# Optimization experiments

Measured on AMD Instinct MI355X. Metric: run time of the kernel, lower is better.

Reference implementation:

```python
import jax, jax.numpy as jnp
import numpy as np

B, T, D, H = 4, 2048, 1024, 8
HD = D // H
RES_SCALE = 1.0 / np.sqrt(2.0 * 2)  # layer_idx = 2


def rmsnorm(x, w, eps=1e-6):
    return w * (x * jax.lax.rsqrt(jnp.mean(x * x, axis=-1, keepdims=True) + eps))


def l2norm(x, eps=1e-6):
    return x * jax.lax.rsqrt(jnp.sum(x * x, axis=-1, keepdims=True) + eps)


def setup_inputs() -> dict:
    key = jax.random.key(0)
    ks = jax.random.split(key, 16)
    s = 0.02
    return {
        'x': jax.random.normal(ks[0], (B, T, D), dtype=jnp.float32),
        'ln1_w': jnp.ones((D,), jnp.float32),
        'qw': jax.random.normal(ks[1], (D, D), jnp.float32) * s,
        'kw': jax.random.normal(ks[2], (D, D), jnp.float32) * s,
        'vw': jax.random.normal(ks[3], (D, D), jnp.float32) * s,
        'bw': jax.random.normal(ks[4], (D, H), jnp.float32) * s,
        'aw': jax.random.normal(ks[5], (D, H), jnp.float32) * s,
        'A_log': jnp.log(jax.random.uniform(ks[6], (H,), jnp.float32, 1.0, 16.0)),
        'dt_bias': jnp.zeros((H,), jnp.float32),
        'gw': jax.random.normal(ks[7], (D, D), jnp.float32) * s,
        'onorm_w': jnp.ones((HD,), jnp.float32),
        'ow': jax.random.normal(ks[8], (D, D), jnp.float32) * s,
        'ln2_w': jnp.ones((D,), jnp.float32),
        'fcw': jax.random.normal(ks[9], (D, 4 * D), jnp.float32) * s,
        'pw': jax.random.normal(ks[10], (4 * D, D), jnp.float32) * s,
    }


def reference(x, ln1_w, qw, kw, vw, bw, aw, A_log, dt_bias, gw, onorm_w, ow, ln2_w, fcw, pw):
    b, t, d = x.shape
    h = rmsnorm(x, ln1_w)
    # projections: SiLU + L2-norm on q/k, SiLU on v (gated delta rule)
    q = l2norm(jax.nn.silu(h @ qw).reshape(b, t, H, HD))
    k = l2norm(jax.nn.silu(h @ kw).reshape(b, t, H, HD))
    v = jax.nn.silu(h @ vw).reshape(b, t, H, HD)
    beta = jax.nn.sigmoid(h @ bw)                                   # [b,t,H]
    g = -jnp.exp(A_log) * jax.nn.softplus(h @ aw + dt_bias)         # [b,t,H] (<=0)

    # time-major for scan
    qs, ks_, vs = (a.transpose(1, 0, 2, 3) for a in (q, k, v))
    bs, gs = beta.transpose(1, 0, 2), g.transpose(1, 0, 2)

    def step(S, inp):
        q_t, k_t, v_t, b_t, g_t = inp
        Sg = jnp.exp(g_t)[..., None, None] * S                      # decay  [b,H,dk,dv]
        kS = jnp.einsum('bhk,bhkv->bhv', k_t, Sg)                   # k^T S
        S = Sg + jnp.einsum('bhk,bhv->bhkv', b_t[..., None] * k_t, v_t - kS)
        o_t = jnp.einsum('bhk,bhkv->bhv', q_t, S)
        return S, o_t

    S0 = jnp.zeros((b, H, HD, HD), x.dtype)
    S_f, os = jax.lax.scan(step, S0, (qs, ks_, vs, bs, gs))
    o = os.transpose(1, 0, 2, 3)                                    # [b,t,H,HD]

    # use_gate: per-head RMSNorm then SiLU output gate
    gate = jax.nn.silu((h @ gw).reshape(b, t, H, HD))
    o = rmsnorm(o, onorm_w) * gate
    o = o.reshape(b, t, d) @ ow

    x1 = x + o * RES_SCALE
    h2 = rmsnorm(x1, ln2_w)
    y = x1 + (jax.nn.silu(h2 @ fcw) @ pw) * RES_SCALE
    return y, S_f
```

## Files before the change

### kernel.cpp

```cpp
#include <hip/hip_runtime.h>
#include <math.h>


#define B_ 4
#define T_ 2048
#define D_ 1024
#define H_ 8
#define HD_ 128
#define RES_SCALE 0.5f

typedef __bf16 bf16x8 __attribute__((ext_vector_type(8)));
typedef float f32x4 __attribute__((ext_vector_type(4)));

__device__ __forceinline__ float bf2f(unsigned short u) {
    union { unsigned int i; float f; } w; w.i = ((unsigned int)u) << 16; return w.f;
}
__device__ __forceinline__ unsigned short f2bf(float f) {
    unsigned int x = __float_as_uint(f);
    x += 0x7fffu + ((x >> 16) & 1u);
    return (unsigned short)(x >> 16);
}
__device__ __forceinline__ float sigm(float x) { return 1.f / (1.f + __expf(-x)); }

__global__ __launch_bounds__(256) void cvt_kernel(const float* __restrict__ src,
                                                  unsigned short* __restrict__ dst, int n4) {
    int i = blockIdx.x * 256 + threadIdx.x;
    if (i < n4) {
        float4 v = ((const float4*)src)[i];
        ushort4 o;
        o.x = f2bf(v.x); o.y = f2bf(v.y); o.z = f2bf(v.z); o.w = f2bf(v.w);
        ((ushort4*)dst)[i] = o;
    }
}

__global__ __launch_bounds__(256) void cvt2_kernel(const float* __restrict__ src,
                                                   unsigned short* __restrict__ hi,
                                                   unsigned short* __restrict__ lo, int n4) {
    int i = blockIdx.x * 256 + threadIdx.x;
    if (i < n4) {
        float4 v = ((const float4*)src)[i];
        ushort4 h, l;
        h.x = f2bf(v.x); l.x = f2bf(v.x - bf2f(h.x));
        h.y = f2bf(v.y); l.y = f2bf(v.y - bf2f(h.y));
        h.z = f2bf(v.z); l.z = f2bf(v.z - bf2f(h.z));
        h.w = f2bf(v.w); l.w = f2bf(v.w - bf2f(h.w));
        ((ushort4*)hi)[i] = h;
        ((ushort4*)lo)[i] = l;
    }
}

__global__ __launch_bounds__(256) void rmsnorm_kernel(const float* __restrict__ x,
                                                      const float* __restrict__ w,
                                                      unsigned short* __restrict__ outh,
                                                      unsigned short* __restrict__ outl) {
    int row = blockIdx.x;
    int tid = threadIdx.x;
    float4 v = ((const float4*)(x + (size_t)row * D_))[tid];
    float ss = v.x * v.x + v.y * v.y + v.z * v.z + v.w * v.w;
    #pragma unroll
    for (int m = 1; m < 64; m <<= 1) ss += __shfl_xor(ss, m);
    __shared__ float red[4];
    if ((tid & 63) == 0) red[tid >> 6] = ss;
    __syncthreads();
    float tot = red[0] + red[1] + red[2] + red[3];
    float sc = rsqrtf(tot * (1.f / D_) + 1e-6f);
    float4 wv = ((const float4*)w)[tid];
    float h0 = v.x * sc * wv.x, h1 = v.y * sc * wv.y;
    float h2 = v.z * sc * wv.z, h3 = v.w * sc * wv.w;
    ushort4 oh;
    oh.x = f2bf(h0); oh.y = f2bf(h1); oh.z = f2bf(h2); oh.w = f2bf(h3);
    ((ushort4*)(outh + (size_t)row * D_))[tid] = oh;
    if (outl) {
        ushort4 ol;
        ol.x = f2bf(h0 - bf2f(oh.x));
        ol.y = f2bf(h1 - bf2f(oh.y));
        ol.z = f2bf(h2 - bf2f(oh.z));
        ol.w = f2bf(h3 - bf2f(oh.w));
        ((ushort4*)(outl + (size_t)row * D_))[tid] = ol;
    }
}

#define LDT 40
__global__ __launch_bounds__(256) void gemm_kernel(const unsigned short* __restrict__ A,
                                                   const unsigned short* __restrict__ Bm,
                                                   unsigned short* __restrict__ Obf,
                                                   float* __restrict__ Of,
                                                   const float* __restrict__ aux,
                                                   int N, int K, int epi) {
    __shared__ unsigned short As[128 * LDT];
    __shared__ unsigned short Bs[128 * LDT];
    int tid = threadIdx.x;
    int lane = tid & 63, wave = tid >> 6;
    int wm = (wave >> 1) * 64, wn = (wave & 1) * 64;
    int l15 = lane & 15, kg = lane >> 4;
    size_t gm = blockIdx.x, gn = blockIdx.y;

    int arow0 = tid >> 2, aseg = (tid & 3) * 8;
    int brow0 = tid >> 4, bc8 = (tid & 15) * 8;

    f32x4 acc[4][4] = {};

    for (int kt = 0; kt < K; kt += 32) {
        uint4 a0 = *(const uint4*)(A + (size_t)(gm * 128 + arow0) * K + kt + aseg);
        uint4 a1 = *(const uint4*)(A + (size_t)(gm * 128 + arow0 + 64) * K + kt + aseg);
        uint4 b0 = *(const uint4*)(Bm + (size_t)(kt + brow0) * N + gn * 128 + bc8);
        uint4 b1 = *(const uint4*)(Bm + (size_t)(kt + brow0 + 16) * N + gn * 128 + bc8);
        __syncthreads();
        *(uint4*)&As[arow0 * LDT + aseg] = a0;
        *(uint4*)&As[(arow0 + 64) * LDT + aseg] = a1;
        {
            unsigned int uu[4] = {b0.x, b0.y, b0.z, b0.w};
            #pragma unroll
            for (int p = 0; p < 4; p++) {
                Bs[(bc8 + 2 * p) * LDT + brow0] = (unsigned short)(uu[p] & 0xffffu);
                Bs[(bc8 + 2 * p + 1) * LDT + brow0] = (unsigned short)(uu[p] >> 16);
            }
            unsigned int vv[4] = {b1.x, b1.y, b1.z, b1.w};
            #pragma unroll
            for (int p = 0; p < 4; p++) {
                Bs[(bc8 + 2 * p) * LDT + brow0 + 16] = (unsigned short)(vv[p] & 0xffffu);
                Bs[(bc8 + 2 * p + 1) * LDT + brow0 + 16] = (unsigned short)(vv[p] >> 16);
            }
        }
        __syncthreads();
        bf16x8 af[4], bfr[4];
        #pragma unroll
        for (int m = 0; m < 4; m++)
            af[m] = *(const bf16x8*)&As[(wm + m * 16 + l15) * LDT + kg * 8];
        #pragma unroll
        for (int n = 0; n < 4; n++)
            bfr[n] = *(const bf16x8*)&Bs[(wn + n * 16 + l15) * LDT + kg * 8];
        #pragma unroll
        for (int m = 0; m < 4; m++)
            #pragma unroll
            for (int n = 0; n < 4; n++)
                acc[m][n] = __builtin_amdgcn_mfma_f32_16x16x32_bf16(af[m], bfr[n], acc[m][n], 0, 0, 0);
    }

    #pragma unroll
    for (int m = 0; m < 4; m++) {
        #pragma unroll
        for (int n = 0; n < 4; n++) {
            #pragma unroll
            for (int j = 0; j < 4; j++) {
                size_t row = gm * 128 + wm + m * 16 + kg * 4 + j;
                size_t col = gn * 128 + wn + n * 16 + l15;
                size_t idx = row * N + col;
                float v = acc[m][n][j];
                if (epi == 0) {
                    Obf[idx] = f2bf(v * sigm(v));
                } else {
                    Of[idx] = aux[idx] + v * RES_SCALE;
                }
            }
        }
    }
}

__global__ __launch_bounds__(256) void gemm32_kernel(const unsigned short* __restrict__ Ah,
                                                     const unsigned short* __restrict__ Al,
                                                     const unsigned short* __restrict__ Bh,
                                                     const unsigned short* __restrict__ Bl,
                                                     float* __restrict__ Of,
                                                     int N, int K) {
    __shared__ unsigned short Ash[128 * LDT];
    __shared__ unsigned short Asl[128 * LDT];
    __shared__ unsigned short Bsh[128 * LDT];
    __shared__ unsigned short Bsl[128 * LDT];
    int tid = threadIdx.x;
    int lane = tid & 63, wave = tid >> 6;
    int wm = (wave >> 1) * 64, wn = (wave & 1) * 64;
    int l15 = lane & 15, kg = lane >> 4;
    size_t gm = blockIdx.x, gn = blockIdx.y;

    int arow0 = tid >> 2, aseg = (tid & 3) * 8;
    int brow0 = tid >> 4, bc8 = (tid & 15) * 8;

    f32x4 acc[4][4] = {};

    for (int kt = 0; kt < K; kt += 32) {
        size_t aoff0 = (size_t)(gm * 128 + arow0) * K + kt + aseg;
        size_t aoff1 = (size_t)(gm * 128 + arow0 + 64) * K + kt + aseg;
        size_t boff0 = (size_t)(kt + brow0) * N + gn * 128 + bc8;
        size_t boff1 = (size_t)(kt + brow0 + 16) * N + gn * 128 + bc8;
        uint4 a0h = *(const uint4*)(Ah + aoff0);
        uint4 a1h = *(const uint4*)(Ah + aoff1);
        uint4 a0l = *(const uint4*)(Al + aoff0);
        uint4 a1l = *(const uint4*)(Al + aoff1);
        uint4 b0h = *(const uint4*)(Bh + boff0);
        uint4 b1h = *(const uint4*)(Bh + boff1);
        uint4 b0l = *(const uint4*)(Bl + boff0);
        uint4 b1l = *(const uint4*)(Bl + boff1);
        __syncthreads();
        *(uint4*)&Ash[arow0 * LDT + aseg] = a0h;
        *(uint4*)&Ash[(arow0 + 64) * LDT + aseg] = a1h;
        *(uint4*)&Asl[arow0 * LDT + aseg] = a0l;
        *(uint4*)&Asl[(arow0 + 64) * LDT + aseg] = a1l;
        {
            unsigned int uu[4];
            uu[0] = b0h.x; uu[1] = b0h.y; uu[2] = b0h.z; uu[3] = b0h.w;
            #pragma unroll
            for (int p = 0; p < 4; p++) {
                Bsh[(bc8 + 2 * p) * LDT + brow0] = (unsigned short)(uu[p] & 0xffffu);
                Bsh[(bc8 + 2 * p + 1) * LDT + brow0] = (unsigned short)(uu[p] >> 16);
            }
            uu[0] = b1h.x; uu[1] = b1h.y; uu[2] = b1h.z; uu[3] = b1h.w;
            #pragma unroll
            for (int p = 0; p < 4; p++) {
                Bsh[(bc8 + 2 * p) * LDT + brow0 + 16] = (unsigned short)(uu[p] & 0xffffu);
                Bsh[(bc8 + 2 * p + 1) * LDT + brow0 + 16] = (unsigned short)(uu[p] >> 16);
            }
            uu[0] = b0l.x; uu[1] = b0l.y; uu[2] = b0l.z; uu[3] = b0l.w;
            #pragma unroll
            for (int p = 0; p < 4; p++) {
                Bsl[(bc8 + 2 * p) * LDT + brow0] = (unsigned short)(uu[p] & 0xffffu);
                Bsl[(bc8 + 2 * p + 1) * LDT + brow0] = (unsigned short)(uu[p] >> 16);
            }
            uu[0] = b1l.x; uu[1] = b1l.y; uu[2] = b1l.z; uu[3] = b1l.w;
            #pragma unroll
            for (int p = 0; p < 4; p++) {
                Bsl[(bc8 + 2 * p) * LDT + brow0 + 16] = (unsigned short)(uu[p] & 0xffffu);
                Bsl[(bc8 + 2 * p + 1) * LDT + brow0 + 16] = (unsigned short)(uu[p] >> 16);
            }
        }
        __syncthreads();
        bf16x8 afh[4], afl[4], bfh[4], bfl[4];
        #pragma unroll
        for (int m = 0; m < 4; m++) {
            afh[m] = *(const bf16x8*)&Ash[(wm + m * 16 + l15) * LDT + kg * 8];
            afl[m] = *(const bf16x8*)&Asl[(wm + m * 16 + l15) * LDT + kg * 8];
        }
        #pragma unroll
        for (int n = 0; n < 4; n++) {
            bfh[n] = *(const bf16x8*)&Bsh[(wn + n * 16 + l15) * LDT + kg * 8];
            bfl[n] = *(const bf16x8*)&Bsl[(wn + n * 16 + l15) * LDT + kg * 8];
        }
        #pragma unroll
        for (int m = 0; m < 4; m++) {
            #pragma unroll
            for (int n = 0; n < 4; n++) {
                acc[m][n] = __builtin_amdgcn_mfma_f32_16x16x32_bf16(afh[m], bfh[n], acc[m][n], 0, 0, 0);
                acc[m][n] = __builtin_amdgcn_mfma_f32_16x16x32_bf16(afh[m], bfl[n], acc[m][n], 0, 0, 0);
                acc[m][n] = __builtin_amdgcn_mfma_f32_16x16x32_bf16(afl[m], bfh[n], acc[m][n], 0, 0, 0);
            }
        }
    }

    #pragma unroll
    for (int m = 0; m < 4; m++) {
        #pragma unroll
        for (int n = 0; n < 4; n++) {
            #pragma unroll
            for (int j = 0; j < 4; j++) {
                size_t row = gm * 128 + wm + m * 16 + kg * 4 + j;
                size_t col = gn * 128 + wn + n * 16 + l15;
                float v = acc[m][n][j];
                Of[row * N + col] = v * sigm(v);
            }
        }
    }
}

__global__ __launch_bounds__(256) void smallproj_kernel(const unsigned short* __restrict__ hh,
                                                        const unsigned short* __restrict__ hl,
                                                        const float* __restrict__ bw,
                                                        const float* __restrict__ aw,
                                                        const float* __restrict__ A_log,
                                                        const float* __restrict__ dt_bias,
                                                        float* __restrict__ beta,
                                                        float* __restrict__ g) {
    int row = blockIdx.x;
    int tid = threadIdx.x;
    int out = tid >> 4, part = tid & 15;
    int head = out & 7;
    const float* W = (out < 8) ? bw : aw;
    const unsigned short* hrh = hh + (size_t)row * D_ + part * 64;
    const unsigned short* hrl = hl + (size_t)row * D_ + part * 64;
    float s = 0.f;
    #pragma unroll
    for (int j8 = 0; j8 < 8; j8++) {
        uint4 uh = *(const uint4*)(hrh + j8 * 8);
        uint4 ul = *(const uint4*)(hrl + j8 * 8);
        unsigned int ah[4] = {uh.x, uh.y, uh.z, uh.w};
        unsigned int al[4] = {ul.x, ul.y, ul.z, ul.w};
        #pragma unroll
        for (int p = 0; p < 4; p++) {
            int k = part * 64 + j8 * 8 + 2 * p;
            float v0 = bf2f((unsigned short)(ah[p] & 0xffffu)) + bf2f((unsigned short)(al[p] & 0xffffu));
            float v1 = bf2f((unsigned short)(ah[p] >> 16)) + bf2f((unsigned short)(al[p] >> 16));
            s += v0 * W[(size_t)k * H_ + head];
            s += v1 * W[(size_t)(k + 1) * H_ + head];
        }
    }
    s += __shfl_xor(s, 1); s += __shfl_xor(s, 2); s += __shfl_xor(s, 4); s += __shfl_xor(s, 8);
    if (part == 0) {
        if (out < 8) {
            beta[(size_t)row * H_ + head] = sigm(s);
        } else {
            float xx = s + dt_bias[head];
            float sp = (xx > 20.f) ? xx : log1pf(expf(xx));
            g[(size_t)row * H_ + head] = -expf(A_log[head]) * sp;
        }
    }
}

__global__ __launch_bounds__(256) void l2norm_kernel(float* __restrict__ qk) {
    int row = blockIdx.x * 4 + (threadIdx.x >> 6);
    int lane = threadIdx.x & 63;
    float* r = qk + (size_t)row * HD_ + lane * 2;
    float2 v = *(const float2*)r;
    float ss = v.x * v.x + v.y * v.y;
    #pragma unroll
    for (int m = 1; m < 64; m <<= 1) ss += __shfl_xor(ss, m);
    float sc = rsqrtf(ss + 1e-6f);
    float2 o = {v.x * sc, v.y * sc};
    *(float2*)r = o;
}

#define CH 32
__global__ __launch_bounds__(512) void scan_kernel(const float* __restrict__ q,
                                                   const float* __restrict__ k,
                                                   const float* __restrict__ v,
                                                   const float* __restrict__ beta,
                                                   const float* __restrict__ g,
                                                   float* __restrict__ o,
                                                   float* __restrict__ Sf) {
    int bh = blockIdx.x >> 1;
    int b = bh >> 3, h = bh & 7;
    int cb = (blockIdx.x & 1) * 64;
    int tid = threadIdx.x;
    int wave = tid >> 6, lane = tid & 63;
    int col = cb + wave * 8 + (lane & 7);
    int oct = lane >> 3;
    int dk0 = oct * 16;

    __shared__ float ks[2][CH][HD_];
    __shared__ float qs[2][CH][HD_];
    __shared__ float vs[2][CH][HD_];
    __shared__ float egs[2][CH];
    __shared__ float bes[2][CH];

    float S[16];
    #pragma unroll
    for (int j = 0; j < 16; j++) S[j] = 0.f;

    int sstep = tid >> 4;
    int sd = (tid & 15) * 8;

    auto stage = [&](int c, int buf) {
        size_t gbase = ((size_t)(b * T_ + c * CH + sstep)) * D_ + h * HD_ + sd;
        float4 q0 = *(const float4*)(q + gbase);
        float4 q1 = *(const float4*)(q + gbase + 4);
        float4 k0 = *(const float4*)(k + gbase);
        float4 k1 = *(const float4*)(k + gbase + 4);
        float4 v0 = *(const float4*)(v + gbase);
        float4 v1 = *(const float4*)(v + gbase + 4);
        *(float4*)&qs[buf][sstep][sd] = q0;
        *(float4*)&qs[buf][sstep][sd + 4] = q1;
        *(float4*)&ks[buf][sstep][sd] = k0;
        *(float4*)&ks[buf][sstep][sd + 4] = k1;
        *(float4*)&vs[buf][sstep][sd] = v0;
        *(float4*)&vs[buf][sstep][sd + 4] = v1;
        if (tid < CH) {
            egs[buf][tid] = expf(g[(size_t)(b * T_ + c * CH + tid) * H_ + h]);
        } else if (tid < 2 * CH) {
            bes[buf][tid - CH] = beta[(size_t)(b * T_ + c * CH + (tid - CH)) * H_ + h];
        }
    };

    auto computeC = [&](int c, int buf) {
        for (int s = 0; s < CH; s++) {
            float eg = egs[buf][s];
            float be = bes[buf][s];
            float vv = vs[buf][s][col];
            float4 kk[4];
            float kr = 0.f;
            #pragma unroll
            for (int j4 = 0; j4 < 4; j4++) {
                kk[j4] = *(const float4*)&ks[buf][s][dk0 + j4 * 4];
                kr += kk[j4].x * S[j4 * 4 + 0] + kk[j4].y * S[j4 * 4 + 1]
                    + kk[j4].z * S[j4 * 4 + 2] + kk[j4].w * S[j4 * 4 + 3];
            }
            kr += __shfl_xor(kr, 8);
            kr += __shfl_xor(kr, 16);
            kr += __shfl_xor(kr, 32);
            float u = be * (vv - eg * kr);
            float4 oa = {0.f, 0.f, 0.f, 0.f};
            #pragma unroll
            for (int j4 = 0; j4 < 4; j4++) {
                float4 q4 = *(const float4*)&qs[buf][s][dk0 + j4 * 4];
                S[j4 * 4 + 0] = eg * S[j4 * 4 + 0] + kk[j4].x * u;
                S[j4 * 4 + 1] = eg * S[j4 * 4 + 1] + kk[j4].y * u;
                S[j4 * 4 + 2] = eg * S[j4 * 4 + 2] + kk[j4].z * u;
                S[j4 * 4 + 3] = eg * S[j4 * 4 + 3] + kk[j4].w * u;
                oa.x += q4.x * S[j4 * 4 + 0];
                oa.y += q4.y * S[j4 * 4 + 1];
                oa.z += q4.z * S[j4 * 4 + 2];
                oa.w += q4.w * S[j4 * 4 + 3];
            }
            float ov = (oa.x + oa.y) + (oa.z + oa.w);
            ov += __shfl_xor(ov, 8);
            ov += __shfl_xor(ov, 16);
            ov += __shfl_xor(ov, 32);
            if (oct == 0) {
                o[((size_t)(b * T_ + c * CH + s)) * D_ + h * HD_ + col] = ov;
            }
        }
    };

    stage(0, 0);
    __syncthreads();
    for (int c = 0; c < T_ / CH; c++) {
        if (c + 1 < T_ / CH) stage(c + 1, (c + 1) & 1);
        computeC(c, c & 1);
        __syncthreads();
    }
    #pragma unroll
    for (int j = 0; j < 16; j++) {
        Sf[((size_t)bh * HD_ + (dk0 + j)) * HD_ + col] = S[j];
    }
}

__global__ __launch_bounds__(256) void gate_kernel(const float* __restrict__ o,
                                                   const unsigned short* __restrict__ gp,
                                                   const float* __restrict__ onw,
                                                   unsigned short* __restrict__ og) {
    int row = blockIdx.x * 4 + (threadIdx.x >> 6);
    int lane = threadIdx.x & 63;
    size_t base = (size_t)row * HD_ + lane * 2;
    float2 v = *(const float2*)(o + base);
    float a = v.x, b = v.y;
    float ss = a * a + b * b;
    #pragma unroll
    for (int m = 1; m < 64; m <<= 1) ss += __shfl_xor(ss, m);
    float sc = rsqrtf(ss * (1.f / HD_) + 1e-6f);
    unsigned int ug = *(const unsigned int*)(gp + base);
    float g0 = bf2f((unsigned short)(ug & 0xffffu)), g1 = bf2f((unsigned short)(ug >> 16));
    float w0 = onw[lane * 2], w1 = onw[lane * 2 + 1];
    float r0 = a * sc * w0 * g0;
    float r1 = b * sc * w1 * g1;
    *(unsigned int*)(og + base) = ((unsigned int)f2bf(r1) << 16) | f2bf(r0);
}

extern "C" void kernel_launch(void* const* d_in, const int* in_sizes, int n_in,
                              void* d_out, int out_size, void* d_ws, size_t ws_size,
                              hipStream_t stream) {
    const float* x = (const float*)d_in[0];
    const float* ln1_w = (const float*)d_in[1];
    const float* qw = (const float*)d_in[2];
    const float* kw = (const float*)d_in[3];
    const float* vw = (const float*)d_in[4];
    const float* bw = (const float*)d_in[5];
    const float* aw = (const float*)d_in[6];
    const float* A_log = (const float*)d_in[7];
    const float* dt_bias = (const float*)d_in[8];
    const float* gw = (const float*)d_in[9];
    const float* onorm_w = (const float*)d_in[10];
    const float* ow = (const float*)d_in[11];
    const float* ln2_w = (const float*)d_in[12];
    const float* fcw = (const float*)d_in[13];
    const float* pw = (const float*)d_in[14];
    float* out = (float*)d_out;

    char* ws = (char*)d_ws;
    const size_t MB = 1024 * 1024;
    unsigned short* WQh = (unsigned short*)(ws + 0 * MB);
    unsigned short* WQl = (unsigned short*)(ws + 2 * MB);
    unsigned short* WKh = (unsigned short*)(ws + 4 * MB);
    unsigned short* WKl = (unsigned short*)(ws + 6 * MB);
    unsigned short* WVh = (unsigned short*)(ws + 8 * MB);
    unsigned short* WVl = (unsigned short*)(ws + 10 * MB);
    unsigned short* WG  = (unsigned short*)(ws + 12 * MB);
    unsigned short* WO  = (unsigned short*)(ws + 14 * MB);
    unsigned short* WFC = (unsigned short*)(ws + 16 * MB);
    unsigned short* WP  = (unsigned short*)(ws + 24 * MB);
    unsigned short* HBh = (unsigned short*)(ws + 32 * MB);
    unsigned short* HBl = (unsigned short*)(ws + 48 * MB);
    float*          QF  = (float*)(ws + 64 * MB);
    float*          KF  = (float*)(ws + 96 * MB);
    float*          VF  = (float*)(ws + 128 * MB);
    unsigned short* GPB = (unsigned short*)(ws + 160 * MB);
    float*          BETA= (float*)(ws + 176 * MB);
    float*          GG  = (float*)(ws + 176 * MB + 262144);
    float*          OF  = (float*)(ws + 177 * MB);
    unsigned short* OGB = (unsigned short*)(ws + 64 * MB);
    float*          X1  = (float*)(ws + 96 * MB);
    unsigned short* H2B = (unsigned short*)(ws + 160 * MB);
    unsigned short* MID = (unsigned short*)(ws + 176 * MB);

    cvt2_kernel<<<1024, 256, 0, stream>>>(qw, WQh, WQl, 262144);
    cvt2_kernel<<<1024, 256, 0, stream>>>(kw, WKh, WKl, 262144);
    cvt2_kernel<<<1024, 256, 0, stream>>>(vw, WVh, WVl, 262144);
    cvt_kernel<<<1024, 256, 0, stream>>>(gw, WG, 262144);
    cvt_kernel<<<1024, 256, 0, stream>>>(ow, WO, 262144);
    cvt_kernel<<<4096, 256, 0, stream>>>(fcw, WFC, 1048576);
    cvt_kernel<<<4096, 256, 0, stream>>>(pw, WP, 1048576);

    rmsnorm_kernel<<<8192, 256, 0, stream>>>(x, ln1_w, HBh, HBl);

    gemm32_kernel<<<dim3(64, 8), 256, 0, stream>>>(HBh, HBl, WQh, WQl, QF, 1024, 1024);
    gemm32_kernel<<<dim3(64, 8), 256, 0, stream>>>(HBh, HBl, WKh, WKl, KF, 1024, 1024);
    gemm32_kernel<<<dim3(64, 8), 256, 0, stream>>>(HBh, HBl, WVh, WVl, VF, 1024, 1024);
    gemm_kernel<<<dim3(64, 8), 256, 0, stream>>>(HBh, WG, GPB, nullptr, nullptr, 1024, 1024, 0);

    smallproj_kernel<<<8192, 256, 0, stream>>>(HBh, HBl, bw, aw, A_log, dt_bias, BETA, GG);

    l2norm_kernel<<<16384, 256, 0, stream>>>(QF);
    l2norm_kernel<<<16384, 256, 0, stream>>>(KF);

    scan_kernel<<<64, 512, 0, stream>>>(QF, KF, VF, BETA, GG, OF, out + 8388608);

    gate_kernel<<<16384, 256, 0, stream>>>(OF, GPB, onorm_w, OGB);

    gemm_kernel<<<dim3(64, 8), 256, 0, stream>>>(OGB, WO, nullptr, X1, x, 1024, 1024, 1);

    rmsnorm_kernel<<<8192, 256, 0, stream>>>(X1, ln2_w, H2B, nullptr);

    gemm_kernel<<<dim3(64, 32), 256, 0, stream>>>(H2B, WFC, MID, nullptr, nullptr, 4096, 1024, 0);

    gemm_kernel<<<dim3(64, 8), 256, 0, stream>>>(MID, WP, nullptr, out, X1, 1024, 4096, 1);
}
```

Baseline: 2.805 ms.

## Fuse QKV and gate projections into one bf16 GEMM, drop split-precision

Replaces the three split-bf16 (hi/lo, 3-MFMA) GEMMs for Q/K/V and the separate gate GEMM with one plain-bf16 GEMM over a concatenated 1024x4096 weight. The concatenated weight is built by a new conversion kernel that writes each matrix into a column slice. The epilogue routes each column block to the Q/K/V float outputs or the bf16 gate buffer. The scan kernel also gets XOR-swizzled shared-memory layouts for q/k and flattened dot products, aimed at fewer bank conflicts. Dropping the lo correction terms cuts MFMA work and memory traffic roughly threefold for these projections, at the cost of lower precision in q/k/v.

```diff
diff --git a/kernel.cpp b/kernel.cpp
--- a/kernel.cpp
+++ b/kernel.cpp
@@ -33,19 +33,16 @@
     }
 }
 
-__global__ __launch_bounds__(256) void cvt2_kernel(const float* __restrict__ src,
-                                                   unsigned short* __restrict__ hi,
-                                                   unsigned short* __restrict__ lo, int n4) {
+__global__ __launch_bounds__(256) void cvtw_kernel(const float* __restrict__ src,
+                                                   unsigned short* __restrict__ dst, int colofs) {
     int i = blockIdx.x * 256 + threadIdx.x;
-    if (i < n4) {
+    if (i < 262144) {
         float4 v = ((const float4*)src)[i];
-        ushort4 h, l;
-        h.x = f2bf(v.x); l.x = f2bf(v.x - bf2f(h.x));
-        h.y = f2bf(v.y); l.y = f2bf(v.y - bf2f(h.y));
-        h.z = f2bf(v.z); l.z = f2bf(v.z - bf2f(h.z));
-        h.w = f2bf(v.w); l.w = f2bf(v.w - bf2f(h.w));
-        ((ushort4*)hi)[i] = h;
-        ((ushort4*)lo)[i] = l;
+        int s4 = i * 4;
+        int srow = s4 >> 10, scol = s4 & 1023;
+        ushort4 o;
+        o.x = f2bf(v.x); o.y = f2bf(v.y); o.z = f2bf(v.z); o.w = f2bf(v.w);
+        *(ushort4*)(dst + (size_t)srow * 4096 + colofs + scol) = o;
     }
 }
 
@@ -157,16 +154,15 @@
     }
 }
 
-__global__ __launch_bounds__(256) void gemm32_kernel(const unsigned short* __restrict__ Ah,
-                                                     const unsigned short* __restrict__ Al,
-                                                     const unsigned short* __restrict__ Bh,
-                                                     const unsigned short* __restrict__ Bl,
-                                                     float* __restrict__ Of,
-                                                     int N, int K) {
-    __shared__ unsigned short Ash[128 * LDT];
-    __shared__ unsigned short Asl[128 * LDT];
-    __shared__ unsigned short Bsh[128 * LDT];
-    __shared__ unsigned short Bsl[128 * LDT];
+__global__ __launch_bounds__(256) void gemm_qkvg_kernel(const unsigned short* __restrict__ A,
+                                                        const unsigned short* __restrict__ Bm,
+                                                        float* __restrict__ Qo,
+                                                        float* __restrict__ Ko,
+                                                        float* __restrict__ Vo,
+                                                        unsigned short* __restrict__ Go) {
+    const int N = 4096, K = 1024;
+    __shared__ unsigned short As[128 * LDT];
+    __shared__ unsigned short Bs[128 * LDT];
     int tid = threadIdx.x;
     int lane = tid & 63, wave = tid >> 6;
     int wm = (wave >> 1) * 64, wn = (wave & 1) * 64;
@@ -179,73 +175,45 @@
     f32x4 acc[4][4] = {};
 
     for (int kt = 0; kt < K; kt += 32) {
-        size_t aoff0 = (size_t)(gm * 128 + arow0) * K + kt + aseg;
-        size_t aoff1 = (size_t)(gm * 128 + arow0 + 64) * K + kt + aseg;
-        size_t boff0 = (size_t)(kt + brow0) * N + gn * 128 + bc8;
-        size_t boff1 = (size_t)(kt + brow0 + 16) * N + gn * 128 + bc8;
-        uint4 a0h = *(const uint4*)(Ah + aoff0);
-        uint4 a1h = *(const uint4*)(Ah + aoff1);
-        uint4 a0l = *(const uint4*)(Al + aoff0);
-        uint4 a1l = *(const uint4*)(Al + aoff1);
-        uint4 b0h = *(const uint4*)(Bh + boff0);
-        uint4 b1h = *(const uint4*)(Bh + boff1);
-        uint4 b0l = *(const uint4*)(Bl + boff0);
-        uint4 b1l = *(const uint4*)(Bl + boff1);
+        uint4 a0 = *(const uint4*)(A + (size_t)(gm * 128 + arow0) * K + kt + aseg);
+        uint4 a1 = *(const uint4*)(A + (size_t)(gm * 128 + arow0 + 64) * K + kt + aseg);
+        uint4 b0 = *(const uint4*)(Bm + (size_t)(kt + brow0) * N + gn * 128 + bc8);
+        uint4 b1 = *(const uint4*)(Bm + (size_t)(kt + brow0 + 16) * N + gn * 128 + bc8);
         __syncthreads();
-        *(uint4*)&Ash[arow0 * LDT + aseg] = a0h;
-        *(uint4*)&Ash[(arow0 + 64) * LDT + aseg] = a1h;
-        *(uint4*)&Asl[arow0 * LDT + aseg] = a0l;
-        *(uint4*)&Asl[(arow0 + 64) * LDT + aseg] = a1l;
+        *(uint4*)&As[arow0 * LDT + aseg] = a0;
+        *(uint4*)&As[(arow0 + 64) * LDT + aseg] = a1;
         {
-            unsigned int uu[4];
-            uu[0] = b0h.x; uu[1] = b0h.y; uu[2] = b0h.z; uu[3] = b0h.w;
+            unsigned int uu[4] = {b0.x, b0.y, b0.z, b0.w};
             #pragma unroll
             for (int p = 0; p < 4; p++) {
-                Bsh[(bc8 + 2 * p) * LDT + brow0] = (unsigned short)(uu[p] & 0xffffu);
-                Bsh[(bc8 + 2 * p + 1) * LDT + brow0] = (unsigned short)(uu[p] >> 16);
-            }
-            uu[0] = b1h.x; uu[1] = b1h.y; uu[2] = b1h.z; uu[3] = b1h.w;
+                Bs[(bc8 + 2 * p) * LDT + brow0] = (unsigned short)(uu[p] & 0xffffu);
+                Bs[(bc8 + 2 * p + 1) * LDT + brow0] = (unsigned short)(uu[p] >> 16);
+            }
+            unsigned int vv[4] = {b1.x, b1.y, b1.z, b1.w};
             #pragma unroll
             for (int p = 0; p < 4; p++) {
-                Bsh[(bc8 + 2 * p) * LDT + brow0 + 16] = (unsigned short)(uu[p] & 0xffffu);
-                Bsh[(bc8 + 2 * p + 1) * LDT + brow0 + 16] = (unsigned short)(uu[p] >> 16);
-            }
-            uu[0] = b0l.x; uu[1] = b0l.y; uu[2] = b0l.z; uu[3] = b0l.w;
-            #pragma unroll
-            for (int p = 0; p < 4; p++) {
-                Bsl[(bc8 + 2 * p) * LDT + brow0] = (unsigned short)(uu[p] & 0xffffu);
-                Bsl[(bc8 + 2 * p + 1) * LDT + brow0] = (unsigned short)(uu[p] >> 16);
-            }
-            uu[0] = b1l.x; uu[1] = b1l.y; uu[2] = b1l.z; uu[3] = b1l.w;
-            #pragma unroll
-            for (int p = 0; p < 4; p++) {
-                Bsl[(bc8 + 2 * p) * LDT + brow0 + 16] = (unsigned short)(uu[p] & 0xffffu);
-                Bsl[(bc8 + 2 * p + 1) * LDT + brow0 + 16] = (unsigned short)(uu[p] >> 16);
+                Bs[(bc8 + 2 * p) * LDT + brow0 + 16] = (unsigned short)(vv[p] & 0xffffu);
+                Bs[(bc8 + 2 * p + 1) * LDT + brow0 + 16] = (unsigned short)(vv[p] >> 16);
             }
         }
         __syncthreads();
-        bf16x8 afh[4], afl[4], bfh[4], bfl[4];
-        #pragma unroll
-        for (int m = 0; m < 4; m++) {
-            afh[m] = *(const bf16x8*)&Ash[(wm + m * 16 + l15) * LDT + kg * 8];
-            afl[m] = *(const bf16x8*)&Asl[(wm + m * 16 + l15) * LDT + kg * 8];
-        }
-        #pragma unroll
-        for (int n = 0; n < 4; n++) {
-            bfh[n] = *(const bf16x8*)&Bsh[(wn + n * 16 + l15) * LDT + kg * 8];
-            bfl[n] = *(const bf16x8*)&Bsl[(wn + n * 16 + l15) * LDT + kg * 8];
-        }
-        #pragma unroll
-        for (int m = 0; m < 4; m++) {
-            #pragma unroll
-            for (int n = 0; n < 4; n++) {
-                acc[m][n] = __builtin_amdgcn_mfma_f32_16x16x32_bf16(afh[m], bfh[n], acc[m][n], 0, 0, 0);
-                acc[m][n] = __builtin_amdgcn_mfma_f32_16x16x32_bf16(afh[m], bfl[n], acc[m][n], 0, 0, 0);
-                acc[m][n] = __builtin_amdgcn_mfma_f32_16x16x32_bf16(afl[m], bfh[n], acc[m][n], 0, 0, 0);
-            }
-        }
-    }
-
+        bf16x8 af[4], bfr[4];
+        #pragma unroll
+        for (int m = 0; m < 4; m++)
+            af[m] = *(const bf16x8*)&As[(wm + m * 16 + l15) * LDT + kg * 8];
+        #pragma unroll
+        for (int n = 0; n < 4; n++)
+            bfr[n] = *(const bf16x8*)&Bs[(wn + n * 16 + l15) * LDT + kg * 8];
+        #pragma unroll
+        for (int m = 0; m < 4; m++)
+            #pragma unroll
+            for (int n = 0; n < 4; n++)
+                acc[m][n] = __builtin_amdgcn_mfma_f32_16x16x32_bf16(af[m], bfr[n], acc[m][n], 0, 0, 0);
+    }
+
+    int sel = (int)(gn >> 3);
+    int colbase = (int)(gn & 7) * 128;
+    float* fo = (sel == 0) ? Qo : (sel == 1) ? Ko : Vo;
     #pragma unroll
     for (int m = 0; m < 4; m++) {
         #pragma unroll
@@ -253,9 +221,11 @@
             #pragma unroll
             for (int j = 0; j < 4; j++) {
                 size_t row = gm * 128 + wm + m * 16 + kg * 4 + j;
-                size_t col = gn * 128 + wn + n * 16 + l15;
+                size_t col = colbase + wn + n * 16 + l15;
                 float v = acc[m][n][j];
-                Of[row * N + col] = v * sigm(v);
+                float s = v * sigm(v);
+                if (sel < 3) fo[row * 1024 + col] = s;
+                else Go[row * 1024 + col] = f2bf(s);
             }
         }
     }
@@ -345,7 +315,17 @@
     for (int j = 0; j < 16; j++) S[j] = 0.f;
 
     int sstep = tid >> 4;
-    int sd = (tid & 15) * 8;
+    int slot0 = (tid & 15) * 2;
+    int sd = slot0 * 4;
+    int sw0 = (slot0 ^ (slot0 >> 3)) << 2;
+    int sw1 = ((slot0 + 1) ^ ((slot0 + 1) >> 3)) << 2;
+
+    int ro[4];
+    #pragma unroll
+    for (int j4 = 0; j4 < 4; j4++) {
+        int sl = oct * 4 + j4;
+        ro[j4] = (sl ^ (sl >> 3)) << 2;
+    }
 
     auto stage = [&](int c, int buf) {
         size_t gbase = ((size_t)(b * T_ + c * CH + sstep)) * D_ + h * HD_ + sd;
@@ -355,10 +335,10 @@
         float4 k1 = *(const float4*)(k + gbase + 4);
         float4 v0 = *(const float4*)(v + gbase);
         float4 v1 = *(const float4*)(v + gbase + 4);
-        *(float4*)&qs[buf][sstep][sd] = q0;
-        *(float4*)&qs[buf][sstep][sd + 4] = q1;
-        *(float4*)&ks[buf][sstep][sd] = k0;
-        *(float4*)&ks[buf][sstep][sd + 4] = k1;
+        *(float4*)&qs[buf][sstep][sw0] = q0;
+        *(float4*)&qs[buf][sstep][sw1] = q1;
+        *(float4*)&ks[buf][sstep][sw0] = k0;
+        *(float4*)&ks[buf][sstep][sw1] = k1;
         *(float4*)&vs[buf][sstep][sd] = v0;
         *(float4*)&vs[buf][sstep][sd + 4] = v1;
         if (tid < CH) {
@@ -373,32 +353,36 @@
             float eg = egs[buf][s];
             float be = bes[buf][s];
             float vv = vs[buf][s][col];
-            float4 kk[4];
-            float kr = 0.f;
-            #pragma unroll
-            for (int j4 = 0; j4 < 4; j4++) {
-                kk[j4] = *(const float4*)&ks[buf][s][dk0 + j4 * 4];
-                kr += kk[j4].x * S[j4 * 4 + 0] + kk[j4].y * S[j4 * 4 + 1]
-                    + kk[j4].z * S[j4 * 4 + 2] + kk[j4].w * S[j4 * 4 + 3];
-            }
+            float4 kk0 = *(const float4*)&ks[buf][s][ro[0]];
+            float4 kk1 = *(const float4*)&ks[buf][s][ro[1]];
+            float4 kk2 = *(const float4*)&ks[buf][s][ro[2]];
+            float4 kk3 = *(const float4*)&ks[buf][s][ro[3]];
+            float4 qq0 = *(const float4*)&qs[buf][s][ro[0]];
+            float4 qq1 = *(const float4*)&qs[buf][s][ro[1]];
+            float4 qq2 = *(const float4*)&qs[buf][s][ro[2]];
+            float4 qq3 = *(const float4*)&qs[buf][s][ro[3]];
+            float p0 = ((kk0.x * S[0] + kk0.y * S[1]) + (kk0.z * S[2] + kk0.w * S[3]));
+            float p1 = ((kk1.x * S[4] + kk1.y * S[5]) + (kk1.z * S[6] + kk1.w * S[7]));
+            float p2 = ((kk2.x * S[8] + kk2.y * S[9]) + (kk2.z * S[10] + kk2.w * S[11]));
+            float p3 = ((kk3.x * S[12] + kk3.y * S[13]) + (kk3.z * S[14] + kk3.w * S[15]));
+            float kr = (p0 + p1) + (p2 + p3);
             kr += __shfl_xor(kr, 8);
             kr += __shfl_xor(kr, 16);
             kr += __shfl_xor(kr, 32);
             float u = be * (vv - eg * kr);
-            float4 oa = {0.f, 0.f, 0.f, 0.f};
-            #pragma unroll
-            for (int j4 = 0; j4 < 4; j4++) {
-                float4 q4 = *(const float4*)&qs[buf][s][dk0 + j4 * 4];
-                S[j4 * 4 + 0] = eg * S[j4 * 4 + 0] + kk[j4].x * u;
-                S[j4 * 4 + 1] = eg * S[j4 * 4 + 1] + kk[j4].y * u;
-                S[j4 * 4 + 2] = eg * S[j4 * 4 + 2] + kk[j4].z * u;
-                S[j4 * 4 + 3] = eg * S[j4 * 4 + 3] + kk[j4].w * u;
-                oa.x += q4.x * S[j4 * 4 + 0];
-                oa.y += q4.y * S[j4 * 4 + 1];
-                oa.z += q4.z * S[j4 * 4 + 2];
-                oa.w += q4.w * S[j4 * 4 + 3];
-            }
-            float ov = (oa.x + oa.y) + (oa.z + oa.w);
+            S[0] = eg * S[0] + kk0.x * u;  S[1] = eg * S[1] + kk0.y * u;
+            S[2] = eg * S[2] + kk0.z * u;  S[3] = eg * S[3] + kk0.w * u;
+            S[4] = eg * S[4] + kk1.x * u;  S[5] = eg * S[5] + kk1.y * u;
+            S[6] = eg * S[6] + kk1.z * u;  S[7] = eg * S[7] + kk1.w * u;
+            S[8] = eg * S[8] + kk2.x * u;  S[9] = eg * S[9] + kk2.y * u;
+            S[10] = eg * S[10] + kk2.z * u; S[11] = eg * S[11] + kk2.w * u;
+            S[12] = eg * S[12] + kk3.x * u; S[13] = eg * S[13] + kk3.y * u;
+            S[14] = eg * S[14] + kk3.z * u; S[15] = eg * S[15] + kk3.w * u;
+            float oa0 = ((qq0.x * S[0] + qq0.y * S[1]) + (qq0.z * S[2] + qq0.w * S[3]));
+            float oa1 = ((qq1.x * S[4] + qq1.y * S[5]) + (qq1.z * S[6] + qq1.w * S[7]));
+            float oa2 = ((qq2.x * S[8] + qq2.y * S[9]) + (qq2.z * S[10] + qq2.w * S[11]));
+            float oa3 = ((qq3.x * S[12] + qq3.y * S[13]) + (qq3.z * S[14] + qq3.w * S[15]));
+            float ov = (oa0 + oa1) + (oa2 + oa3);
             ov += __shfl_xor(ov, 8);
             ov += __shfl_xor(ov, 16);
             ov += __shfl_xor(ov, 32);
@@ -464,44 +448,35 @@
 
     char* ws = (char*)d_ws;
     const size_t MB = 1024 * 1024;
-    unsigned short* WQh = (unsigned short*)(ws + 0 * MB);
-    unsigned short* WQl = (unsigned short*)(ws + 2 * MB);
-    unsigned short* WKh = (unsigned short*)(ws + 4 * MB);
-    unsigned short* WKl = (unsigned short*)(ws + 6 * MB);
-    unsigned short* WVh = (unsigned short*)(ws + 8 * MB);
-    unsigned short* WVl = (unsigned short*)(ws + 10 * MB);
-    unsigned short* WG  = (unsigned short*)(ws + 12 * MB);
-    unsigned short* WO  = (unsigned short*)(ws + 14 * MB);
-    unsigned short* WFC = (unsigned short*)(ws + 16 * MB);
-    unsigned short* WP  = (unsigned short*)(ws + 24 * MB);
-    unsigned short* HBh = (unsigned short*)(ws + 32 * MB);
-    unsigned short* HBl = (unsigned short*)(ws + 48 * MB);
-    float*          QF  = (float*)(ws + 64 * MB);
-    float*          KF  = (float*)(ws + 96 * MB);
-    float*          VF  = (float*)(ws + 128 * MB);
-    unsigned short* GPB = (unsigned short*)(ws + 160 * MB);
-    float*          BETA= (float*)(ws + 176 * MB);
-    float*          GG  = (float*)(ws + 176 * MB + 262144);
-    float*          OF  = (float*)(ws + 177 * MB);
-    unsigned short* OGB = (unsigned short*)(ws + 64 * MB);
-    float*          X1  = (float*)(ws + 96 * MB);
-    unsigned short* H2B = (unsigned short*)(ws + 160 * MB);
-    unsigned short* MID = (unsigned short*)(ws + 176 * MB);
-
-    cvt2_kernel<<<1024, 256, 0, stream>>>(qw, WQh, WQl, 262144);
-    cvt2_kernel<<<1024, 256, 0, stream>>>(kw, WKh, WKl, 262144);
-    cvt2_kernel<<<1024, 256, 0, stream>>>(vw, WVh, WVl, 262144);
-    cvt_kernel<<<1024, 256, 0, stream>>>(gw, WG, 262144);
+    unsigned short* WALL = (unsigned short*)(ws + 0 * MB);
+    unsigned short* WO   = (unsigned short*)(ws + 8 * MB);
+    unsigned short* WFC  = (unsigned short*)(ws + 10 * MB);
+    unsigned short* WP   = (unsigned short*)(ws + 18 * MB);
+    unsigned short* HBh = (unsigned short*)(ws + 26 * MB);
+    unsigned short* HBl = (unsigned short*)(ws + 42 * MB);
+    float*          QF  = (float*)(ws + 58 * MB);
+    float*          KF  = (float*)(ws + 90 * MB);
+    float*          VF  = (float*)(ws + 122 * MB);
+    unsigned short* GPB = (unsigned short*)(ws + 154 * MB);
+    float*          BETA= (float*)(ws + 170 * MB);
+    float*          GG  = (float*)(ws + 170 * MB + 262144);
+    float*          OF  = (float*)(ws + 171 * MB);
+    unsigned short* OGB = (unsigned short*)(ws + 58 * MB);
+    float*          X1  = (float*)(ws + 90 * MB);
+    unsigned short* H2B = (unsigned short*)(ws + 154 * MB);
+    unsigned short* MID = (unsigned short*)(ws + 171 * MB);
+
+    cvtw_kernel<<<1024, 256, 0, stream>>>(qw, WALL, 0);
+    cvtw_kernel<<<1024, 256, 0, stream>>>(kw, WALL, 1024);
+    cvtw_kernel<<<1024, 256, 0, stream>>>(vw, WALL, 2048);
+    cvtw_kernel<<<1024, 256, 0, stream>>>(gw, WALL, 3072);
     cvt_kernel<<<1024, 256, 0, stream>>>(ow, WO, 262144);
     cvt_kernel<<<4096, 256, 0, stream>>>(fcw, WFC, 1048576);
     cvt_kernel<<<4096, 256, 0, stream>>>(pw, WP, 1048576);
 
     rmsnorm_kernel<<<8192, 256, 0, stream>>>(x, ln1_w, HBh, HBl);
 
-    gemm32_kernel<<<dim3(64, 8), 256, 0, stream>>>(HBh, HBl, WQh, WQl, QF, 1024, 1024);
-    gemm32_kernel<<<dim3(64, 8), 256, 0, stream>>>(HBh, HBl, WKh, WKl, KF, 1024, 1024);
-    gemm32_kernel<<<dim3(64, 8), 256, 0, stream>>>(HBh, HBl, WVh, WVl, VF, 1024, 1024);
-    gemm_kernel<<<dim3(64, 8), 256, 0, stream>>>(HBh, WG, GPB, nullptr, nullptr, 1024, 1024, 0);
+    gemm_qkvg_kernel<<<dim3(64, 32), 256, 0, stream>>>(HBh, WALL, QF, KF, VF, GPB);
 
     smallproj_kernel<<<8192, 256, 0, stream>>>(HBh, HBl, bw, aw, A_log, dt_bias, BETA, GG);
 
```

After: 2.546 ms. -9.2%, faster.
